# Performance work log

Measured on AMD Instinct MI355X. Metric: run time of the kernel, lower is better.

Reference implementation:

```python
import jax, jax.numpy as jnp
import numpy as np

N, E, G, B = 50000, 1600000, 128, 128
FP = 33     # num_feature_pro
ED = 128    # embed_dim
ML = 3000   # max_len


def setup_inputs() -> dict:
    key = jax.random.key(0)
    ks = jax.random.split(key, 20)
    s = lambda k, shape: jax.random.normal(k, shape, jnp.float32) * 0.02
    inp = {}
    inp["pro_x"] = jax.random.normal(ks[0], (N, FP), jnp.float32)
    inp["edge_index"] = jax.random.randint(ks[1], (2, E), 0, N)
    inp["edge_weight"] = jax.random.uniform(ks[2], (E,), jnp.float32)
    inp["pro_batch"] = jnp.sort(jax.random.randint(ks[3], (N,), 0, G))
    inp["rna_global"] = jax.random.randint(ks[4], (B, ML), 0, 5)
    inp["rna_local"] = jax.random.randint(ks[5], (B, ML - 2), 0, 65)
    inp["emb1"] = s(ks[6], (5, ED))
    inp["emb2"] = s(ks[7], (65, ED))
    inp["convW1"] = s(ks[8], (32, ML, 8));     inp["convb1"] = jnp.zeros((32,), jnp.float32)
    inp["convW2"] = s(ks[9], (32, ML - 2, 8)); inp["convb2"] = jnp.zeros((32,), jnp.float32)
    inp["fcxr_W"] = s(ks[10], (32 * 121, 128)); inp["fcxr_b"] = jnp.zeros((128,), jnp.float32)
    inp["gcn1_W"] = s(ks[11], (FP, FP));         inp["gcn1_b"] = jnp.zeros((FP,), jnp.float32)
    inp["gcn2_W"] = s(ks[12], (FP, 2 * FP));     inp["gcn2_b"] = jnp.zeros((2 * FP,), jnp.float32)
    inp["gcn3_W"] = s(ks[13], (2 * FP, 4 * FP)); inp["gcn3_b"] = jnp.zeros((4 * FP,), jnp.float32)
    inp["bn1_g"] = jnp.ones((FP,), jnp.float32);     inp["bn1_b"] = jnp.zeros((FP,), jnp.float32)
    inp["bn2_g"] = jnp.ones((2 * FP,), jnp.float32); inp["bn2_b"] = jnp.zeros((2 * FP,), jnp.float32)
    inp["bn3_g"] = jnp.ones((4 * FP,), jnp.float32); inp["bn3_b"] = jnp.zeros((4 * FP,), jnp.float32)
    inp["fcg1_W"] = s(ks[14], (4 * FP, 1024)); inp["fcg1_b"] = jnp.zeros((1024,), jnp.float32)
    inp["fcg2_W"] = s(ks[15], (1024, 128));    inp["fcg2_b"] = jnp.zeros((128,), jnp.float32)
    return inp


def _gcn(x, W, b, src, dst, ew, n):
    # PyG GCNConv: x' = D^{-1/2}(A+I)D^{-1/2} (x W) + b, self-loop weight 1
    xw = x @ W                                           # [n, out]
    deg = jax.ops.segment_sum(ew, dst, num_segments=n) + 1.0
    dis = jax.lax.rsqrt(deg)
    norm = dis[src] * ew * dis[dst]                      # [E]
    out = jax.ops.segment_sum(xw[src] * norm[:, None], dst, num_segments=n)
    out = out + xw * (dis * dis)[:, None]                # self loops
    return out + b


def _bn(x, g, b, eps=1e-5):
    # NodeLevelBatchNorm (training): batch stats over the node dim, biased var
    m = x.mean(0)
    v = ((x - m) ** 2).mean(0)
    return (x - m) * jax.lax.rsqrt(v + eps) * g + b


def _conv1d(x, W, b):
    # x: [B, C, L], W: [O, C, K] -> [B, O, L-K+1]
    y = jax.lax.conv_general_dilated(x, W, (1,), 'VALID',
                                     dimension_numbers=('NCH', 'OIH', 'NCH'))
    return y + b[None, :, None]


def _rna(tok, emb, cW, cb, fW, fb):
    e = emb[tok]                     # [B, seq, 128] -> channels=seq, length=128
    y = _conv1d(e, cW, cb)           # [B, 32, 121]
    return y.reshape(y.shape[0], -1) @ fW + fb


def reference(pro_x, edge_index, edge_weight, pro_batch, rna_global, rna_local,
              emb1, emb2, convW1, convb1, convW2, convb2, fcxr_W, fcxr_b,
              gcn1_W, gcn1_b, gcn2_W, gcn2_b, gcn3_W, gcn3_b,
              bn1_g, bn1_b, bn2_g, bn2_b, bn3_g, bn3_b,
              fcg1_W, fcg1_b, fcg2_W, fcg2_b):
    src, dst = edge_index[0], edge_index[1]
    n = pro_x.shape[0]
    # RNA branch (fc_xr shared between global and local)
    xrg = _rna(rna_global, emb1, convW1, convb1, fcxr_W, fcxr_b)
    xrl = _rna(rna_local, emb2, convW2, convb2, fcxr_W, fcxr_b)
    # Protein GCN branch
    xp = jax.nn.relu(_bn(_gcn(pro_x, gcn1_W, gcn1_b, src, dst, edge_weight, n), bn1_g, bn1_b))
    ones = jnp.ones_like(edge_weight)
    xp = jax.nn.relu(_bn(_gcn(xp, gcn2_W, gcn2_b, src, dst, ones, n), bn2_g, bn2_b))
    xp = jax.nn.relu(_bn(_gcn(xp, gcn3_W, gcn3_b, src, dst, ones, n), bn3_g, bn3_b))
    # global mean pool per graph
    cnt = jax.ops.segment_sum(jnp.ones((n,), xp.dtype), pro_batch, num_segments=G)
    pooled = jax.ops.segment_sum(xp, pro_batch, num_segments=G) / jnp.maximum(cnt, 1.0)[:, None]
    h = jax.nn.relu(pooled @ fcg1_W + fcg1_b)
    xp_out = h @ fcg2_W + fcg2_b     # dropout = identity (eval)
    xc_rna = (xrg + xrl) * 0.5       # mean over stacked [xrg, xrl]
    return (xc_rna, xp_out)
```

## Files before the change

kernel.cpp:

```cpp
#include <hip/hip_runtime.h>
#include <hip/hip_bf16.h>

typedef __hip_bfloat16 bf16;

#define NN 50000
#define NE 1600000
#define NG 128
#define NB 128
#define SG 3000
#define SL 2998
#define VG 5
#define VL 65
#define EDB 6250
#define AGB 12500
#define NA  (NB*VG + NB*VL)
#define NGB (32*VG + 32*VL)
#define CASTB ((NN*40+255)/256)

__device__ __forceinline__ float b2f(bf16 x){ return __bfloat162float(x); }
__device__ __forceinline__ float blo(unsigned u){ return __uint_as_float(u << 16); }
__device__ __forceinline__ float bhi(unsigned u){ return __uint_as_float(u & 0xffff0000u); }

__global__ void k_front(const int* __restrict__ rna_g, const int* __restrict__ rna_l,
                        int* __restrict__ tcnt_g, int* __restrict__ toff_g,
                        int* __restrict__ bucket_g,
                        int* __restrict__ tcnt_l, int* __restrict__ toff_l,
                        int* __restrict__ bucket_l,
                        const float* __restrict__ convW1, const float* __restrict__ convW2,
                        float* __restrict__ Wr1, float* __restrict__ Wr2,
                        const float* __restrict__ fcxrW, const float* __restrict__ cb1,
                        const float* __restrict__ cb2, float* __restrict__ bias0,
                        const int* __restrict__ dst, const float* __restrict__ ew,
                        double* __restrict__ packed, int* __restrict__ slot){
    int bx = blockIdx.x;
    int t = threadIdx.x;
    if (bx < 2*NB){
        __shared__ int hist[VL], pre[VL], cur[VL];
        int br = bx & 1, b = bx >> 1;
        const int* tok = br ? rna_l : rna_g;
        int S = br ? SL : SG, V = br ? VL : VG;
        int* tcnt = br ? tcnt_l : tcnt_g;
        int* toff = br ? toff_l : toff_g;
        int* bucket = br ? bucket_l : bucket_g;
        if (t < V) hist[t] = 0;
        __syncthreads();
        for (int i = t; i < S; i += 256) atomicAdd(&hist[tok[b*S + i]], 1);
        __syncthreads();
        if (t == 0){
            int run = 0;
            for (int v = 0; v < V; ++v){ pre[v] = run; run += hist[v]; }
        }
        __syncthreads();
        if (t < V){
            tcnt[b*V + t] = hist[t];
            toff[b*V + t] = pre[t];
            cur[t] = pre[t];
        }
        __syncthreads();
        for (int i = t; i < S; i += 256){
            int v = tok[b*S + i];
            int p = atomicAdd(&cur[v], 1);
            bucket[b*S + p] = i;
        }
        return;
    }
    bx -= 2*NB;
    if (bx < EDB){
        int e = bx*256 + t;
        double old = unsafeAtomicAdd(&packed[dst[e]], 1048576.0 + (double)ew[e]);
        slot[e] = (int)(old * (1.0/1048576.0));
        return;
    }
    bx -= EDB;
    if (bx < SG + SL){
        const float* W; float* Wr; int S, c = bx;
        if (c < SG){ W = convW1; Wr = Wr1; S = SG; }
        else { c -= SG; W = convW2; Wr = Wr2; S = SL; }
        Wr[c*256 + t] = W[((t >> 3)*S + c)*8 + (t & 7)];
        return;
    }
    bx -= SG + SL;
    if (t >= 128) return;
    int o = bx, j = t;
    float s = 0.f;
    const float* Wo = fcxrW + o*121*128 + j;
    for (int l = 0; l < 121; ++l) s += Wo[l*128];
    unsafeAtomicAdd(&bias0[j], 0.5f * (cb1[o] + cb2[o]) * s);
}

__device__ void dev_buildA(const float* __restrict__ Wr, const int* __restrict__ bucket,
                           const int* __restrict__ toff, const int* __restrict__ tcnt,
                           float* __restrict__ A, int S, int V, int bv){
    int b = bv / V, v = bv - b*V;
    int t = threadIdx.x;
    const int* bk = bucket + b*S + toff[b*V + v];
    int m = tcnt[b*V + v];
    float acc = 0.f;
    int idx = 0;
    for (; idx + 4 <= m; idx += 4){
        int c0 = bk[idx], c1 = bk[idx+1], c2 = bk[idx+2], c3 = bk[idx+3];
        acc += Wr[c0*256 + t];
        acc += Wr[c1*256 + t];
        acc += Wr[c2*256 + t];
        acc += Wr[c3*256 + t];
    }
    for (; idx < m; ++idx) acc += Wr[bk[idx]*256 + t];
    A[b*(256*V) + v*256 + t] = acc;
}

__global__ void k_F1(const float* __restrict__ Wr1, const float* __restrict__ Wr2,
                     const int* __restrict__ bucket_g, const int* __restrict__ toff_g,
                     const int* __restrict__ tcnt_g, float* __restrict__ Ag,
                     const int* __restrict__ bucket_l, const int* __restrict__ toff_l,
                     const int* __restrict__ tcnt_l, float* __restrict__ Al,
                     const double* __restrict__ packed, int* __restrict__ cnt,
                     float2* __restrict__ dis12, float2* __restrict__ self12,
                     const int* __restrict__ batch, int* __restrict__ gstart,
                     int* __restrict__ bsum,
                     const float* __restrict__ fcxrb, const float* __restrict__ bias0,
                     float* __restrict__ out0){
    __shared__ int sd[256];
    int bx = blockIdx.x;
    if (bx < NA){
        if (bx < NB*VG) dev_buildA(Wr1, bucket_g, toff_g, tcnt_g, Ag, SG, VG, bx);
        else dev_buildA(Wr2, bucket_l, toff_l, tcnt_l, Al, SL, VL, bx - NB*VG);
        return;
    }
    bx -= NA;
    int t = threadIdx.x;
    if (bx == 49){
        for (int idx = t; idx < NB*128; idx += 256)
            out0[idx] = fcxrb[idx & 127] + bias0[idx & 127];
        return;
    }
    int base = bx*1024;
    int s = 0;
    #pragma unroll
    for (int j = 0; j < 4; ++j){
        int i = base + t*4 + j;
        if (i < NN){
            double p = packed[i];
            int c = (int)(p * (1.0/1048576.0));
            float w = (float)(p - (double)c * 1048576.0);
            cnt[i] = c; s += c;
            float r1 = rsqrtf(w + 1.0f);
            float r2 = rsqrtf((float)c + 1.0f);
            dis12[i] = make_float2(r1, r2);
            self12[i] = make_float2(r1*r1, r2*r2);
            int pb = batch[i];
            int prev = (i == 0) ? -1 : batch[i-1];
            for (int g = prev + 1; g <= pb; ++g) gstart[g] = i;
            if (i == NN - 1){
                for (int g = pb + 1; g <= NG; ++g) gstart[g] = NN;
            }
        }
    }
    sd[t] = s; __syncthreads();
    for (int d = 128; d > 0; d >>= 1){
        if (t < d) sd[t] += sd[t+d];
        __syncthreads();
    }
    if (t == 0) bsum[bx] = sd[0];
}

__global__ void k_scan3(const int* __restrict__ cnt, const int* __restrict__ bsum,
                        int* __restrict__ offs){
    __shared__ int sd[256];
    __shared__ int sbase;
    int t = threadIdx.x;
    if (t == 0){
        int run = 0;
        for (int i = 0; i < blockIdx.x; ++i) run += bsum[i];
        sbase = run;
    }
    int base = blockIdx.x*1024;
    int loc[4]; int s = 0;
    #pragma unroll
    for (int j = 0; j < 4; ++j){
        int idx = base + t*4 + j;
        loc[j] = (idx < NN) ? cnt[idx] : 0;
        s += loc[j];
    }
    sd[t] = s; __syncthreads();
    for (int d = 1; d < 256; d <<= 1){
        int v = (t >= d) ? sd[t-d] : 0;
        __syncthreads();
        sd[t] += v;
        __syncthreads();
    }
    int run = sbase + (sd[t] - s);
    #pragma unroll
    for (int j = 0; j < 4; ++j){
        int idx = base + t*4 + j;
        if (idx < NN) offs[idx] = run;
        run += loc[j];
    }
}

__device__ void dev_buildG(float (*rows)[128], const float* __restrict__ emb,
                           const float* __restrict__ W, bf16* __restrict__ G,
                           int V, int q){
    int o = q / V, mt = q - o*V;
    int t = threadIdx.x;
    int j = t & 127, half = t >> 7;
    int kk[4], vv[4];
    #pragma unroll
    for (int qq = 0; qq < 4; ++qq){
        int mm = half*4 + qq;
        int m = mt*8 + mm;
        int k = m / V, v = m - k*V;
        kk[qq] = k; vv[qq] = v;
        rows[mm][j] = emb[v*128 + j];
    }
    __syncthreads();
    float a0=0.f, a1=0.f, a2=0.f, a3=0.f;
    const float* Wo = W + o*121*128 + j;
    for (int l = 0; l < 121; ++l){
        float w = Wo[l*128];
        a0 += rows[half*4+0][l + kk[0]] * w;
        a1 += rows[half*4+1][l + kk[1]] * w;
        a2 += rows[half*4+2][l + kk[2]] * w;
        a3 += rows[half*4+3][l + kk[3]] * w;
    }
    float a[4] = {a0, a1, a2, a3};
    #pragma unroll
    for (int qq = 0; qq < 4; ++qq){
        int row = vv[qq]*256 + o*8 + kk[qq];
        G[(size_t)row*128 + j] = __float2bfloat16(a[qq]);
    }
}

__global__ void k_F2(const int* __restrict__ src, const int* __restrict__ dst,
                     const float* __restrict__ ew, const float2* __restrict__ dis12,
                     const int* __restrict__ offs, const int* __restrict__ slot,
                     float4* __restrict__ epk,
                     const float* __restrict__ emb1, const float* __restrict__ emb2,
                     const float* __restrict__ fcxrW, bf16* __restrict__ G1,
                     bf16* __restrict__ G2,
                     const float* __restrict__ pro_x, bf16* __restrict__ xb0){
    __shared__ float rows[8][128];
    int bx = blockIdx.x;
    if (bx < 32*VG){ dev_buildG(rows, emb1, fcxrW, G1, VG, bx); return; }
    if (bx < NGB){ dev_buildG(rows, emb2, fcxrW, G2, VL, bx - 32*VG); return; }
    bx -= NGB;
    if (bx < EDB){
        int e = bx*256 + threadIdx.x;
        int s = src[e], d = dst[e];
        int pos = offs[d] + slot[e];
        float2 a = dis12[s], b = dis12[d];
        float4 v;
        v.x = __int_as_float(s*80);
        v.y = a.x * ew[e] * b.x;
        v.z = a.y * b.y;
        v.w = __int_as_float(s*144);
        epk[pos] = v;
        return;
    }
    bx -= EDB;
    int i = bx*256 + threadIdx.x;
    if (i >= NN*40) return;
    int n = i / 40, f = i - n*40;
    xb0[i] = __float2bfloat16(f < 33 ? pro_x[n*33 + f] : 0.f);
}

template<int QV, int GRP, int OFF_W, int N_Z>
__device__ void dev_agg(float* sAgg ,
                        const bf16* __restrict__ xb, const float4* __restrict__ epk,
                        const int* __restrict__ offs, const int* __restrict__ cnt,
                        const float2* __restrict__ self12,
                        const float* __restrict__ W, const float* __restrict__ bias,
                        float* __restrict__ tout, float* __restrict__ bnpart,
                        int F, int OF, int bx){
    const int LPG = 64 / GRP;
    int wave = threadIdx.x >> 6;
    int node = bx*4 + wave;
    int lane = threadIdx.x & 63;
    int grp  = lane / LPG;
    int gl   = lane % LPG;
    bool act = gl < QV;
    const char* xc = (const char*)xb;
    float a0=0,a1=0,a2=0,a3=0,a4=0,a5=0,a6=0,a7=0;
    int b = offs[node], e = b + cnt[node];
    if (act){
        int fo = gl << 4;
        if (grp == 0){
            float2 sw2 = self12[node];
            float sw = N_Z ? sw2.y : sw2.x;
            uint4 u = *(const uint4*)(xc + node*(QV*16) + fo);
            a0 = sw*blo(u.x); a1 = sw*bhi(u.x); a2 = sw*blo(u.y); a3 = sw*bhi(u.y);
            a4 = sw*blo(u.z); a5 = sw*bhi(u.z); a6 = sw*blo(u.w); a7 = sw*bhi(u.w);
        }
        int p = b + grp;
        for (; p + 3*GRP < e; p += 4*GRP){
            float4 e0 = epk[p];
            float4 e1 = epk[p +   GRP];
            float4 e2 = epk[p + 2*GRP];
            float4 e3 = epk[p + 3*GRP];
            int o0 = __float_as_int(OFF_W ? e0.w : e0.x); float n0 = N_Z ? e0.z : e0.y;
            int o1 = __float_as_int(OFF_W ? e1.w : e1.x); float n1 = N_Z ? e1.z : e1.y;
            int o2 = __float_as_int(OFF_W ? e2.w : e2.x); float n2 = N_Z ? e2.z : e2.y;
            int o3 = __float_as_int(OFF_W ? e3.w : e3.x); float n3 = N_Z ? e3.z : e3.y;
            uint4 u0 = *(const uint4*)(xc + o0 + fo);
            uint4 u1 = *(const uint4*)(xc + o1 + fo);
            uint4 u2 = *(const uint4*)(xc + o2 + fo);
            uint4 u3 = *(const uint4*)(xc + o3 + fo);
            a0 += n0*blo(u0.x); a1 += n0*bhi(u0.x); a2 += n0*blo(u0.y); a3 += n0*bhi(u0.y);
            a4 += n0*blo(u0.z); a5 += n0*bhi(u0.z); a6 += n0*blo(u0.w); a7 += n0*bhi(u0.w);
            a0 += n1*blo(u1.x); a1 += n1*bhi(u1.x); a2 += n1*blo(u1.y); a3 += n1*bhi(u1.y);
            a4 += n1*blo(u1.z); a5 += n1*bhi(u1.z); a6 += n1*blo(u1.w); a7 += n1*bhi(u1.w);
            a0 += n2*blo(u2.x); a1 += n2*bhi(u2.x); a2 += n2*blo(u2.y); a3 += n2*bhi(u2.y);
            a4 += n2*blo(u2.z); a5 += n2*bhi(u2.z); a6 += n2*blo(u2.w); a7 += n2*bhi(u2.w);
            a0 += n3*blo(u3.x); a1 += n3*bhi(u3.x); a2 += n3*blo(u3.y); a3 += n3*bhi(u3.y);
            a4 += n3*blo(u3.z); a5 += n3*bhi(u3.z); a6 += n3*blo(u3.w); a7 += n3*bhi(u3.w);
        }
        if (p < e){
            int p1 = p + GRP, p2 = p + 2*GRP;
            bool v1 = p1 < e, v2 = p2 < e;
            float4 e0 = epk[p];
            float4 e1 = epk[v1 ? p1 : p];
            float4 e2 = epk[v2 ? p2 : p];
            int o0 = __float_as_int(OFF_W ? e0.w : e0.x);
            int o1 = __float_as_int(OFF_W ? e1.w : e1.x);
            int o2 = __float_as_int(OFF_W ? e2.w : e2.x);
            float n0 = N_Z ? e0.z : e0.y;
            float n1 = v1 ? (N_Z ? e1.z : e1.y) : 0.f;
            float n2 = v2 ? (N_Z ? e2.z : e2.y) : 0.f;
            uint4 u0 = *(const uint4*)(xc + o0 + fo);
            uint4 u1 = *(const uint4*)(xc + o1 + fo);
            uint4 u2 = *(const uint4*)(xc + o2 + fo);
            a0 += n0*blo(u0.x); a1 += n0*bhi(u0.x); a2 += n0*blo(u0.y); a3 += n0*bhi(u0.y);
            a4 += n0*blo(u0.z); a5 += n0*bhi(u0.z); a6 += n0*blo(u0.w); a7 += n0*bhi(u0.w);
            a0 += n1*blo(u1.x); a1 += n1*bhi(u1.x); a2 += n1*blo(u1.y); a3 += n1*bhi(u1.y);
            a4 += n1*blo(u1.z); a5 += n1*bhi(u1.z); a6 += n1*blo(u1.w); a7 += n1*bhi(u1.w);
            a0 += n2*blo(u2.x); a1 += n2*bhi(u2.x); a2 += n2*blo(u2.y); a3 += n2*bhi(u2.y);
            a4 += n2*blo(u2.z); a5 += n2*bhi(u2.z); a6 += n2*blo(u2.w); a7 += n2*bhi(u2.w);
        }
    }
    #pragma unroll
    for (int m = LPG; m < 64; m <<= 1){
        a0 += __shfl_xor(a0, m); a1 += __shfl_xor(a1, m);
        a2 += __shfl_xor(a2, m); a3 += __shfl_xor(a3, m);
        a4 += __shfl_xor(a4, m); a5 += __shfl_xor(a5, m);
        a6 += __shfl_xor(a6, m); a7 += __shfl_xor(a7, m);
    }
    if (act && grp == 0){
        float4* dst = (float4*)&sAgg[wave*(QV*8) + gl*8];
        dst[0] = make_float4(a0, a1, a2, a3);
        dst[1] = make_float4(a4, a5, a6, a7);
    }
    __syncthreads();
    int i0 = bx*4;
    int j = threadIdx.x;
    if (j < OF){
        float c0 = bias[j], c1 = c0, c2 = c0, c3 = c0;
        const float* Wj = W + j;
        const float* s0 = sAgg;
        const float* s1 = sAgg + QV*8;
        const float* s2 = sAgg + 2*QV*8;
        const float* s3 = sAgg + 3*QV*8;
        #pragma unroll 4
        for (int f = 0; f < F; ++f){
            float w = Wj[f*OF];
            c0 += s0[f]*w; c1 += s1[f]*w; c2 += s2[f]*w; c3 += s3[f]*w;
        }
        tout[(size_t)(i0+0)*OF + j] = c0;
        tout[(size_t)(i0+1)*OF + j] = c1;
        tout[(size_t)(i0+2)*OF + j] = c2;
        tout[(size_t)(i0+3)*OF + j] = c3;
        float s  = c0 + c1 + c2 + c3;
        float ss = c0*c0 + c1*c1 + c2*c2 + c3*c3;
        float* part = bnpart + (bx & 63)*(2*OF);
        unsafeAtomicAdd(&part[j], s);
        unsafeAtomicAdd(&part[OF + j], ss);
    }
}

template<int QV, int GRP, int OFF_W, int N_Z>
__global__ void k_agg_gemm(const bf16* __restrict__ xb, const float4* __restrict__ epk,
                           const int* __restrict__ offs, const int* __restrict__ cnt,
                           const float2* __restrict__ self12,
                           const float* __restrict__ W, const float* __restrict__ bias,
                           float* __restrict__ tout, float* __restrict__ bnpart,
                           int F, int OF){
    __shared__ float sAgg[4*QV*8];
    dev_agg<QV,GRP,OFF_W,N_Z>(sAgg, xb, epk, offs, cnt, self12, W, bias,
                              tout, bnpart, F, OF, blockIdx.x);
}

__device__ void dev_gemmR(float* xs , int bq,
                          const float* __restrict__ Ag, const bf16* __restrict__ G1,
                          const float* __restrict__ Al, const bf16* __restrict__ G2,
                          float* __restrict__ out0){
    int kpart = bq >> 4;
    int bgrp  = bq & 15;
    const float* X; const bf16* G; int K, k0;
    if (kpart < 5){ X = Ag; G = G1; K = 1280;  k0 = kpart*256; }
    else          { X = Al; G = G2; K = 16640; k0 = (kpart-5)*256; }
    int b0 = bgrp*8;
    int t = threadIdx.x;
    #pragma unroll
    for (int i = 0; i < 8; ++i)
        xs[i*256 + t] = X[(b0+i)*K + k0 + t];
    __syncthreads();
    int rq = t >> 7, j = t & 127;
    const float* x0 = xs + (rq*4)*256;
    float a0=0,a1=0,a2=0,a3=0;
    const bf16* Gp = G + (size_t)k0*128 + j;
    for (int kk = 0; kk < 256; ++kk){
        float g = b2f(Gp[kk*128]);
        a0 += x0[kk]*g; a1 += x0[256+kk]*g; a2 += x0[512+kk]*g; a3 += x0[768+kk]*g;
    }
    unsafeAtomicAdd(&out0[(b0+rq*4+0)*128 + j], 0.5f*a0);
    unsafeAtomicAdd(&out0[(b0+rq*4+1)*128 + j], 0.5f*a1);
    unsafeAtomicAdd(&out0[(b0+rq*4+2)*128 + j], 0.5f*a2);
    unsafeAtomicAdd(&out0[(b0+rq*4+3)*128 + j], 0.5f*a3);
}

__global__ void k_L3(const bf16* __restrict__ xb, const float4* __restrict__ epk,
                     const int* __restrict__ offs, const int* __restrict__ cnt,
                     const float2* __restrict__ self12,
                     const float* __restrict__ W, const float* __restrict__ bias,
                     float* __restrict__ tout, float* __restrict__ bnpart,
                     const float* __restrict__ Ag, const bf16* __restrict__ G1,
                     const float* __restrict__ Al, const bf16* __restrict__ G2,
                     float* __restrict__ out0){
    __shared__ float smem[8*256];
    int bx = blockIdx.x;
    if (bx < AGB){
        dev_agg<9,4,1,1>(smem, xb, epk, offs, cnt, self12, W, bias, tout, bnpart,
                         66, 132, bx);
    } else {
        dev_gemmR(smem, bx - AGB, Ag, G1, Al, G2, out0);
    }
}

__global__ void k_bn_fin(const float* __restrict__ part, float* __restrict__ sums, int OF){
    int tid = threadIdx.x;
    if (tid >= 2*OF) return;
    float s = 0.f;
    #pragma unroll 8
    for (int k = 0; k < 64; ++k) s += part[k*(2*OF) + tid];
    sums[tid] = s;
}

__global__ void k_bn_apply(const float* __restrict__ t, const float* __restrict__ sums,
                           const float* __restrict__ g, const float* __restrict__ b,
                           bf16* __restrict__ xo, int OF, int OS, int total){
    int id = blockIdx.x*256 + threadIdx.x;
    if (id >= total) return;
    int i = id / OS, f = id - i*OS;
    float v = 0.f;
    if (f < OF){
        float m  = sums[f] * (1.0f/(float)NN);
        float vr = sums[OF + f] * (1.0f/(float)NN) - m*m;
        float sc = g[f] * rsqrtf(vr + 1e-5f);
        float sh = b[f] - m*sc;
        v = t[(size_t)i*OF + f] * sc + sh;
        v = v > 0.f ? v : 0.f;
    }
    xo[id] = __float2bfloat16(v);
}

__global__ void k_poolBN(const float* __restrict__ t, const float* __restrict__ sums,
                         const float* __restrict__ g, const float* __restrict__ b,
                         const int* __restrict__ gstart, float* __restrict__ poolsum){
    int gr = blockIdx.x, strip = blockIdx.y, f = threadIdx.x;
    if (f >= 132) return;
    float m  = sums[f] * (1.0f/(float)NN);
    float vr = sums[132 + f] * (1.0f/(float)NN) - m*m;
    float sc = g[f] * rsqrtf(vr + 1e-5f);
    float sh = b[f] - m*sc;
    int i0 = gstart[gr], i1 = gstart[gr+1];
    float s = 0.f;
    for (int i = i0 + strip; i < i1; i += 4){
        float v = t[(size_t)i*132 + f] * sc + sh;
        s += v > 0.f ? v : 0.f;
    }
    unsafeAtomicAdd(&poolsum[gr*132 + f], s);
}

__global__ void k_fcgF(const float* __restrict__ poolsum, const int* __restrict__ gstart,
                       const float* __restrict__ W1, const float* __restrict__ b1,
                       const float* __restrict__ W2, const float* __restrict__ b2,
                       float* __restrict__ out){
    __shared__ float pr[132];
    __shared__ float hr[1024];
    __shared__ float part[8][128];
    int g = blockIdx.x, t = threadIdx.x;
    if (t < 132){
        float inv = 1.0f / fmaxf((float)(gstart[g+1] - gstart[g]), 1.0f);
        pr[t] = poolsum[g*132 + t] * inv;
    }
    __syncthreads();
    float acc = b1[t];
    #pragma unroll 4
    for (int f = 0; f < 132; ++f) acc += pr[f] * W1[f*1024 + t];
    hr[t] = acc > 0.f ? acc : 0.f;
    __syncthreads();
    int ks = t >> 7, j = t & 127;
    const float* Wp = W2 + (ks*128)*128 + j;
    const float* hp = hr + ks*128;
    float a = 0.f;
    #pragma unroll 8
    for (int kk = 0; kk < 128; ++kk) a += hp[kk] * Wp[(size_t)kk*128];
    part[ks][j] = a;
    __syncthreads();
    if (t < 128){
        float s = b2[t];
        #pragma unroll
        for (int r = 0; r < 8; ++r) s += part[r][t];
        out[g*128 + t] = s;
    }
}

extern "C" void kernel_launch(void* const* d_in, const int* in_sizes, int n_in,
                              void* d_out, int out_size, void* d_ws, size_t ws_size,
                              hipStream_t stream)
{
    (void)in_sizes; (void)n_in; (void)out_size; (void)ws_size;

    const float* pro_x  = (const float*)d_in[0];
    const int*   eidx   = (const int*)  d_in[1];
    const float* ew     = (const float*)d_in[2];
    const int*   pbatch = (const int*)  d_in[3];
    const int*   rna_g  = (const int*)  d_in[4];
    const int*   rna_l  = (const int*)  d_in[5];
    const float* emb1   = (const float*)d_in[6];
    const float* emb2   = (const float*)d_in[7];
    const float* convW1 = (const float*)d_in[8];
    const float* convb1 = (const float*)d_in[9];
    const float* convW2 = (const float*)d_in[10];
    const float* convb2 = (const float*)d_in[11];
    const float* fcxrW  = (const float*)d_in[12];
    const float* fcxrb  = (const float*)d_in[13];
    const float* g1W = (const float*)d_in[14];
    const float* g1b = (const float*)d_in[15];
    const float* g2W = (const float*)d_in[16];
    const float* g2b = (const float*)d_in[17];
    const float* g3W = (const float*)d_in[18];
    const float* g3b = (const float*)d_in[19];
    const float* bn1g = (const float*)d_in[20];
    const float* bn1b = (const float*)d_in[21];
    const float* bn2g = (const float*)d_in[22];
    const float* bn2b = (const float*)d_in[23];
    const float* bn3g = (const float*)d_in[24];
    const float* bn3b = (const float*)d_in[25];
    const float* fcg1W = (const float*)d_in[26];
    const float* fcg1b = (const float*)d_in[27];
    const float* fcg2W = (const float*)d_in[28];
    const float* fcg2b = (const float*)d_in[29];

    const int* e_src = eidx;
    const int* e_dst = eidx + NE;

    char* base = (char*)d_ws;
    size_t off = 0;
    auto alloc = [&](size_t bytes)->char*{
        off = (off + 255) & ~(size_t)255;
        char* p = base + off; off += bytes; return p;
    };

    double* packed  = (double*)alloc(NN*8);
    float* bnsum1  = (float*)alloc(2*33*4);
    float* bnsum2  = (float*)alloc(2*66*4);
    float* bnsum3  = (float*)alloc(2*132*4);
    float* poolsum = (float*)alloc(NG*132*4);
    float* bias0   = (float*)alloc(128*4);
    float* bnpart1 = (float*)alloc(64*2*33*4);
    float* bnpart2 = (float*)alloc(64*2*66*4);
    float* bnpart3 = (float*)alloc(64*2*132*4);
    size_t zero_bytes = (off + 255) & ~(size_t)255;

    int*    cnt    = (int*)   alloc(NN*4);
    float2* dis12  = (float2*)alloc(NN*8);
    float2* self12 = (float2*)alloc(NN*8);
    int*    offs   = (int*)   alloc(NN*4);
    int*    bsum   = (int*)   alloc(64*4);
    int*    gstart = (int*)   alloc((NG+1)*4);
    float4* epk    = (float4*)alloc((size_t)NE*16);
    float*  bufB   = (float*) alloc((size_t)NN*132*4);
    bf16*   xbA    = (bf16*)  alloc((size_t)NE*4);
    bf16*   xbB    = (bf16*)  alloc((size_t)NN*72*2);
    float*  Ag     = (float*) alloc((size_t)NB*256*VG*4);
    float*  Al     = (float*) alloc((size_t)NB*256*VL*4);
    bf16*   G1     = (bf16*)  alloc((size_t)32*8*VG*128*2);
    bf16*   G2     = (bf16*)  alloc((size_t)32*8*VL*128*2);

    int*  slot = (int*)xbA;
    bf16* xb0  = (bf16*)xbB;

    float* out0 = (float*)d_out;
    float* out1 = (float*)d_out + 16384;

    char* rb = (char*)bufB;
    size_t ro = 0;
    auto ralloc = [&](size_t bytes)->char*{
        ro = (ro + 255) & ~(size_t)255;
        char* p = rb + ro; ro += bytes; return p;
    };
    int* toff_g   = (int*)ralloc(NB*VG*4);
    int* toff_l   = (int*)ralloc(NB*VL*4);
    int* tcnt_g   = (int*)ralloc(NB*VG*4);
    int* tcnt_l   = (int*)ralloc(NB*VL*4);
    int* bucket_g = (int*)ralloc((size_t)NB*SG*4);
    int* bucket_l = (int*)ralloc((size_t)NB*SL*4);
    float* Wr1    = (float*)ralloc((size_t)SG*256*4);
    float* Wr2    = (float*)ralloc((size_t)SL*256*4);

    hipMemsetAsync(d_ws, 0, zero_bytes, stream);

    k_front<<<2*NB + EDB + SG + SL + 32, 256, 0, stream>>>(
        rna_g, rna_l, tcnt_g, toff_g, bucket_g, tcnt_l, toff_l, bucket_l,
        convW1, convW2, Wr1, Wr2, fcxrW, convb1, convb2, bias0,
        e_dst, ew, packed, slot);

    k_F1<<<NA + 50, 256, 0, stream>>>(Wr1, Wr2,
                                      bucket_g, toff_g, tcnt_g, Ag,
                                      bucket_l, toff_l, tcnt_l, Al,
                                      packed, cnt, dis12, self12, pbatch, gstart,
                                      bsum, fcxrb, bias0, out0);
    k_scan3<<<49, 256, 0, stream>>>(cnt, bsum, offs);

    k_F2<<<NGB + EDB + CASTB, 256, 0, stream>>>(
        e_src, e_dst, ew, dis12, offs, slot, epk,
        emb1, emb2, fcxrW, G1, G2, pro_x, xb0);

    k_agg_gemm<5,8,0,0><<<AGB, 256, 0, stream>>>(xb0, epk, offs, cnt, self12,
                                                 g1W, g1b, bufB, bnpart1, 33, 33);
    k_bn_fin<<<1, 512, 0, stream>>>(bnpart1, bnsum1, 33);
    k_bn_apply<<<(NN*40+255)/256, 256, 0, stream>>>(bufB, bnsum1, bn1g, bn1b,
                                                    xbA, 33, 40, NN*40);

    k_agg_gemm<5,8,0,1><<<AGB, 256, 0, stream>>>(xbA, epk, offs, cnt, self12,
                                                 g2W, g2b, bufB, bnpart2, 33, 66);
    k_bn_fin<<<1, 512, 0, stream>>>(bnpart2, bnsum2, 66);
    k_bn_apply<<<(NN*72+255)/256, 256, 0, stream>>>(bufB, bnsum2, bn2g, bn2b,
                                                    xbB, 66, 72, NN*72);

    k_L3<<<AGB + 1120, 256, 0, stream>>>(xbB, epk, offs, cnt, self12,
                                         g3W, g3b, bufB, bnpart3, Ag, G1, Al, G2, out0);
    k_bn_fin<<<1, 512, 0, stream>>>(bnpart3, bnsum3, 132);

    k_poolBN<<<dim3(NG,4), 192, 0, stream>>>(bufB, bnsum3, bn3g, bn3b, gstart, poolsum);
    k_fcgF<<<NG, 1024, 0, stream>>>(poolsum, gstart, fcg1W, fcg1b, fcg2W, fcg2b, out1);
}
```

Baseline: 571.5 us.

## Fuse BN finalize into consumers, merge pooling into FC kernel, shrink partials

Result: slower. 656.7 us (+14.9%).

```diff
diff --git a/kernel.cpp b/kernel.cpp
--- a/kernel.cpp
+++ b/kernel.cpp
@@ -2,6 +2,7 @@
 #include <hip/hip_bf16.h>
 
 typedef __hip_bfloat16 bf16;
+typedef unsigned short u16;
 
 #define NN 50000
 #define NE 1600000
@@ -16,6 +17,7 @@
 #define NA  (NB*VG + NB*VL)
 #define NGB (32*VG + 32*VL)
 #define CASTB ((NN*40+255)/256)
+#define NSTR 8
 
 __device__ __forceinline__ float b2f(bf16 x){ return __bfloat162float(x); }
 __device__ __forceinline__ float blo(unsigned u){ return __uint_as_float(u << 16); }
@@ -23,9 +25,9 @@
 
 __global__ void k_front(const int* __restrict__ rna_g, const int* __restrict__ rna_l,
                         int* __restrict__ tcnt_g, int* __restrict__ toff_g,
-                        int* __restrict__ bucket_g,
+                        u16* __restrict__ bucket_g,
                         int* __restrict__ tcnt_l, int* __restrict__ toff_l,
-                        int* __restrict__ bucket_l,
+                        u16* __restrict__ bucket_l,
                         const float* __restrict__ convW1, const float* __restrict__ convW2,
                         float* __restrict__ Wr1, float* __restrict__ Wr2,
                         const float* __restrict__ fcxrW, const float* __restrict__ cb1,
@@ -41,7 +43,7 @@
         int S = br ? SL : SG, V = br ? VL : VG;
         int* tcnt = br ? tcnt_l : tcnt_g;
         int* toff = br ? toff_l : toff_g;
-        int* bucket = br ? bucket_l : bucket_g;
+        u16* bucket = br ? bucket_l : bucket_g;
         if (t < V) hist[t] = 0;
         __syncthreads();
         for (int i = t; i < S; i += 256) atomicAdd(&hist[tok[b*S + i]], 1);
@@ -60,7 +62,7 @@
         for (int i = t; i < S; i += 256){
             int v = tok[b*S + i];
             int p = atomicAdd(&cur[v], 1);
-            bucket[b*S + p] = i;
+            bucket[b*S + p] = (u16)i;
         }
         return;
     }
@@ -88,12 +90,12 @@
     unsafeAtomicAdd(&bias0[j], 0.5f * (cb1[o] + cb2[o]) * s);
 }
 
-__device__ void dev_buildA(const float* __restrict__ Wr, const int* __restrict__ bucket,
+__device__ void dev_buildA(const float* __restrict__ Wr, const u16* __restrict__ bucket,
                            const int* __restrict__ toff, const int* __restrict__ tcnt,
                            float* __restrict__ A, int S, int V, int bv){
     int b = bv / V, v = bv - b*V;
     int t = threadIdx.x;
-    const int* bk = bucket + b*S + toff[b*V + v];
+    const u16* bk = bucket + b*S + toff[b*V + v];
     int m = tcnt[b*V + v];
     float acc = 0.f;
     int idx = 0;
@@ -109,9 +111,9 @@
 }
 
 __global__ void k_F1(const float* __restrict__ Wr1, const float* __restrict__ Wr2,
-                     const int* __restrict__ bucket_g, const int* __restrict__ toff_g,
+                     const u16* __restrict__ bucket_g, const int* __restrict__ toff_g,
                      const int* __restrict__ tcnt_g, float* __restrict__ Ag,
-                     const int* __restrict__ bucket_l, const int* __restrict__ toff_l,
+                     const u16* __restrict__ bucket_l, const int* __restrict__ toff_l,
                      const int* __restrict__ tcnt_l, float* __restrict__ Al,
                      const double* __restrict__ packed, int* __restrict__ cnt,
                      float2* __restrict__ dis12, float2* __restrict__ self12,
@@ -369,19 +371,20 @@
         tout[(size_t)(i0+3)*OF + j] = c3;
         float s  = c0 + c1 + c2 + c3;
         float ss = c0*c0 + c1*c1 + c2*c2 + c3*c3;
-        float* part = bnpart + (bx & 63)*(2*OF);
+        float* part = bnpart + (bx & (NSTR-1))*(2*OF);
         unsafeAtomicAdd(&part[j], s);
         unsafeAtomicAdd(&part[OF + j], ss);
     }
 }
 
 template<int QV, int GRP, int OFF_W, int N_Z>
-__global__ void k_agg_gemm(const bf16* __restrict__ xb, const float4* __restrict__ epk,
-                           const int* __restrict__ offs, const int* __restrict__ cnt,
-                           const float2* __restrict__ self12,
-                           const float* __restrict__ W, const float* __restrict__ bias,
-                           float* __restrict__ tout, float* __restrict__ bnpart,
-                           int F, int OF){
+__global__ __launch_bounds__(256, 8)
+void k_agg_gemm(const bf16* __restrict__ xb, const float4* __restrict__ epk,
+                const int* __restrict__ offs, const int* __restrict__ cnt,
+                const float2* __restrict__ self12,
+                const float* __restrict__ W, const float* __restrict__ bias,
+                float* __restrict__ tout, float* __restrict__ bnpart,
+                int F, int OF){
     __shared__ float sAgg[4*QV*8];
     dev_agg<QV,GRP,OFF_W,N_Z>(sAgg, xb, epk, offs, cnt, self12, W, bias,
                               tout, bnpart, F, OF, blockIdx.x);
@@ -434,25 +437,25 @@
     }
 }
 
-__global__ void k_bn_fin(const float* __restrict__ part, float* __restrict__ sums, int OF){
-    int tid = threadIdx.x;
-    if (tid >= 2*OF) return;
-    float s = 0.f;
-    #pragma unroll 8
-    for (int k = 0; k < 64; ++k) s += part[k*(2*OF) + tid];
-    sums[tid] = s;
-}
-
-__global__ void k_bn_apply(const float* __restrict__ t, const float* __restrict__ sums,
+__global__ void k_bn_apply(const float* __restrict__ t, const float* __restrict__ part,
                            const float* __restrict__ g, const float* __restrict__ b,
                            bf16* __restrict__ xo, int OF, int OS, int total){
-    int id = blockIdx.x*256 + threadIdx.x;
+    __shared__ float fs[264];
+    int tid = threadIdx.x;
+    for (int i = tid; i < 2*OF; i += 256){
+        float s = 0.f;
+        #pragma unroll
+        for (int k = 0; k < NSTR; ++k) s += part[k*(2*OF) + i];
+        fs[i] = s;
+    }
+    __syncthreads();
+    int id = blockIdx.x*256 + tid;
     if (id >= total) return;
     int i = id / OS, f = id - i*OS;
     float v = 0.f;
     if (f < OF){
-        float m  = sums[f] * (1.0f/(float)NN);
-        float vr = sums[OF + f] * (1.0f/(float)NN) - m*m;
+        float m  = fs[f] * (1.0f/(float)NN);
+        float vr = fs[OF + f] * (1.0f/(float)NN) - m*m;
         float sc = g[f] * rsqrtf(vr + 1e-5f);
         float sh = b[f] - m*sc;
         v = t[(size_t)i*OF + f] * sc + sh;
@@ -461,40 +464,56 @@
     xo[id] = __float2bfloat16(v);
 }
 
-__global__ void k_poolBN(const float* __restrict__ t, const float* __restrict__ sums,
-                         const float* __restrict__ g, const float* __restrict__ b,
-                         const int* __restrict__ gstart, float* __restrict__ poolsum){
-    int gr = blockIdx.x, strip = blockIdx.y, f = threadIdx.x;
-    if (f >= 132) return;
-    float m  = sums[f] * (1.0f/(float)NN);
-    float vr = sums[132 + f] * (1.0f/(float)NN) - m*m;
-    float sc = g[f] * rsqrtf(vr + 1e-5f);
-    float sh = b[f] - m*sc;
-    int i0 = gstart[gr], i1 = gstart[gr+1];
-    float s = 0.f;
-    for (int i = i0 + strip; i < i1; i += 4){
-        float v = t[(size_t)i*132 + f] * sc + sh;
-        s += v > 0.f ? v : 0.f;
-    }
-    unsafeAtomicAdd(&poolsum[gr*132 + f], s);
-}
-
-__global__ void k_fcgF(const float* __restrict__ poolsum, const int* __restrict__ gstart,
+__global__ void k_fcgF(const float* __restrict__ bufB, const float* __restrict__ part3,
+                       const float* __restrict__ bn3g, const float* __restrict__ bn3b,
+                       const int* __restrict__ gstart,
                        const float* __restrict__ W1, const float* __restrict__ b1,
                        const float* __restrict__ W2, const float* __restrict__ b2,
                        float* __restrict__ out){
+    __shared__ float fs[264];
+    __shared__ float scs[132], shs[132];
+    __shared__ float pp[7][132];
     __shared__ float pr[132];
     __shared__ float hr[1024];
     __shared__ float part[8][128];
     int g = blockIdx.x, t = threadIdx.x;
+    for (int i = t; i < 264; i += 1024){
+        float s = 0.f;
+        #pragma unroll
+        for (int k = 0; k < NSTR; ++k) s += part3[k*264 + i];
+        fs[i] = s;
+    }
+    __syncthreads();
     if (t < 132){
-        float inv = 1.0f / fmaxf((float)(gstart[g+1] - gstart[g]), 1.0f);
-        pr[t] = poolsum[g*132 + t] * inv;
+        float m  = fs[t] * (1.0f/(float)NN);
+        float vr = fs[132 + t] * (1.0f/(float)NN) - m*m;
+        float sc = bn3g[t] * rsqrtf(vr + 1e-5f);
+        scs[t] = sc;
+        shs[t] = bn3b[t] - m*sc;
+    }
+    __syncthreads();
+    int i0 = gstart[g], i1 = gstart[g+1];
+    int r = t / 132, f = t - r*132;
+    if (r < 7){
+        float acc = 0.f;
+        for (int i = i0 + r; i < i1; i += 7){
+            float v = bufB[(size_t)i*132 + f] * scs[f] + shs[f];
+            acc += v > 0.f ? v : 0.f;
+        }
+        pp[r][f] = acc;
+    }
+    __syncthreads();
+    if (t < 132){
+        float s = 0.f;
+        #pragma unroll
+        for (int k = 0; k < 7; ++k) s += pp[k][t];
+        float inv = 1.0f / fmaxf((float)(i1 - i0), 1.0f);
+        pr[t] = s * inv;
     }
     __syncthreads();
     float acc = b1[t];
     #pragma unroll 4
-    for (int f = 0; f < 132; ++f) acc += pr[f] * W1[f*1024 + t];
+    for (int ff = 0; ff < 132; ++ff) acc += pr[ff] * W1[ff*1024 + t];
     hr[t] = acc > 0.f ? acc : 0.f;
     __syncthreads();
     int ks = t >> 7, j = t & 127;
@@ -508,7 +527,7 @@
     if (t < 128){
         float s = b2[t];
         #pragma unroll
-        for (int r = 0; r < 8; ++r) s += part[r][t];
+        for (int rr = 0; rr < 8; ++rr) s += part[rr][t];
         out[g*128 + t] = s;
     }
 }
@@ -561,14 +580,10 @@
     };
 
     double* packed  = (double*)alloc(NN*8);
-    float* bnsum1  = (float*)alloc(2*33*4);
-    float* bnsum2  = (float*)alloc(2*66*4);
-    float* bnsum3  = (float*)alloc(2*132*4);
-    float* poolsum = (float*)alloc(NG*132*4);
     float* bias0   = (float*)alloc(128*4);
-    float* bnpart1 = (float*)alloc(64*2*33*4);
-    float* bnpart2 = (float*)alloc(64*2*66*4);
-    float* bnpart3 = (float*)alloc(64*2*132*4);
+    float* bnpart1 = (float*)alloc(NSTR*2*33*4);
+    float* bnpart2 = (float*)alloc(NSTR*2*66*4);
+    float* bnpart3 = (float*)alloc(NSTR*2*132*4);
     size_t zero_bytes = (off + 255) & ~(size_t)255;
 
     int*    cnt    = (int*)   alloc(NN*4);
@@ -602,8 +617,8 @@
     int* toff_l   = (int*)ralloc(NB*VL*4);
     int* tcnt_g   = (int*)ralloc(NB*VG*4);
     int* tcnt_l   = (int*)ralloc(NB*VL*4);
-    int* bucket_g = (int*)ralloc((size_t)NB*SG*4);
-    int* bucket_l = (int*)ralloc((size_t)NB*SL*4);
+    u16* bucket_g = (u16*)ralloc((size_t)NB*SG*2);
+    u16* bucket_l = (u16*)ralloc((size_t)NB*SL*2);
     float* Wr1    = (float*)ralloc((size_t)SG*256*4);
     float* Wr2    = (float*)ralloc((size_t)SL*256*4);
 
@@ -627,20 +642,17 @@
 
     k_agg_gemm<5,8,0,0><<<AGB, 256, 0, stream>>>(xb0, epk, offs, cnt, self12,
                                                  g1W, g1b, bufB, bnpart1, 33, 33);
-    k_bn_fin<<<1, 512, 0, stream>>>(bnpart1, bnsum1, 33);
-    k_bn_apply<<<(NN*40+255)/256, 256, 0, stream>>>(bufB, bnsum1, bn1g, bn1b,
+    k_bn_apply<<<(NN*40+255)/256, 256, 0, stream>>>(bufB, bnpart1, bn1g, bn1b,
                                                     xbA, 33, 40, NN*40);
 
     k_agg_gemm<5,8,0,1><<<AGB, 256, 0, stream>>>(xbA, epk, offs, cnt, self12,
                                                  g2W, g2b, bufB, bnpart2, 33, 66);
-    k_bn_fin<<<1, 512, 0, stream>>>(bnpart2, bnsum2, 66);
-    k_bn_apply<<<(NN*72+255)/256, 256, 0, stream>>>(bufB, bnsum2, bn2g, bn2b,
+    k_bn_apply<<<(NN*72+255)/256, 256, 0, stream>>>(bufB, bnpart2, bn2g, bn2b,
                                                     xbB, 66, 72, NN*72);
 
     k_L3<<<AGB + 1120, 256, 0, stream>>>(xbB, epk, offs, cnt, self12,
                                          g3W, g3b, bufB, bnpart3, Ag, G1, Al, G2, out0);
-    k_bn_fin<<<1, 512, 0, stream>>>(bnpart3, bnsum3, 132);
-
-    k_poolBN<<<dim3(NG,4), 192, 0, stream>>>(bufB, bnsum3, bn3g, bn3b, gstart, poolsum);
-    k_fcgF<<<NG, 1024, 0, stream>>>(poolsum, gstart, fcg1W, fcg1b, fcg2W, fcg2b, out1);
-}
+
+    k_fcgF<<<NG, 1024, 0, stream>>>(bufB, bnpart3, bn3g, bn3b, gstart,
+                                    fcg1W, fcg1b, fcg2W, fcg2b, out1);
+}
```
